# Kernel tuning notes

Hardware: AMD Instinct MI355X
Metric: run time of the kernel (lower is better)

Reference implementation:

```python
import jax, jax.numpy as jnp
import numpy as np

N = 100000
E = 1600000
IN_F = 128
HIDDEN = 128
HEADS = 2
N_CLASSES = 40
NEG_SLOPE = 0.2
BN_EPS = 1e-5


def setup_inputs() -> dict:
    key = jax.random.key(0)
    ks = jax.random.split(key, 12)
    c1 = HIDDEN // HEADS  # 64
    c2 = N_CLASSES        # 40 per head, concat=False
    inp = {
        "x": jax.random.normal(ks[0], (N, IN_F), dtype=jnp.float32),
        "edge_index": jax.random.randint(ks[1], (2, E), 0, N, dtype=jnp.int32),
        # layer 1 GATConv params
        "W1": jax.random.normal(ks[2], (IN_F, HEADS * c1), dtype=jnp.float32) * 0.05,
        "att_src1": jax.random.normal(ks[3], (HEADS, c1), dtype=jnp.float32) * 0.05,
        "att_dst1": jax.random.normal(ks[4], (HEADS, c1), dtype=jnp.float32) * 0.05,
        "b1": jnp.zeros((HEADS * c1,), dtype=jnp.float32),
        # BatchNorm params
        "gamma": jnp.ones((HIDDEN,), dtype=jnp.float32),
        "beta": jnp.zeros((HIDDEN,), dtype=jnp.float32),
        # layer 2 GATConv params (concat=False)
        "W2": jax.random.normal(ks[5], (HIDDEN, HEADS * c2), dtype=jnp.float32) * 0.05,
        "att_src2": jax.random.normal(ks[6], (HEADS, c2), dtype=jnp.float32) * 0.05,
        "att_dst2": jax.random.normal(ks[7], (HEADS, c2), dtype=jnp.float32) * 0.05,
        "b2": jnp.zeros((c2,), dtype=jnp.float32),
    }
    return inp


def gat_conv(x, src, dst, W, att_src, att_dst, bias, heads, concat):
    n = x.shape[0]
    h = (x @ W).reshape(n, heads, -1)             # [N, H, C]
    a_src = jnp.sum(h * att_src[None], axis=-1)   # [N, H]
    a_dst = jnp.sum(h * att_dst[None], axis=-1)   # [N, H]
    alpha = jax.nn.leaky_relu(a_src[src] + a_dst[dst], NEG_SLOPE)  # [E, H]
    # numerically-stable segment softmax over edges grouped by dst
    amax = jax.ops.segment_max(alpha, dst, num_segments=n)
    e = jnp.exp(alpha - amax[dst])
    denom = jax.ops.segment_sum(e, dst, num_segments=n)
    w = e / denom[dst]                            # [E, H]
    msg = h[src] * w[:, :, None]                  # [E, H, C]
    out = jax.ops.segment_sum(msg, dst, num_segments=n)  # [N, H, C]
    if concat:
        out = out.reshape(n, -1)
    else:
        out = out.mean(axis=1)
    return out + bias


def batch_norm(x, gamma, beta):
    mean = x.mean(axis=0)
    var = x.var(axis=0)
    return (x - mean) * jax.lax.rsqrt(var + BN_EPS) * gamma + beta


def reference(x, edge_index, W1, att_src1, att_dst1, b1, gamma, beta,
              W2, att_src2, att_dst2, b2):
    n = x.shape[0]
    # PyG GATConv default: add self-loops
    loops = jnp.arange(n, dtype=edge_index.dtype)
    src = jnp.concatenate([edge_index[0], loops])
    dst = jnp.concatenate([edge_index[1], loops])
    h = gat_conv(x, src, dst, W1, att_src1, att_dst1, b1, HEADS, concat=True)
    h = batch_norm(h, gamma, beta)
    h = gat_conv(h, src, dst, W2, att_src2, att_dst2, b2, HEADS, concat=False)
    return jax.nn.log_softmax(h, axis=1)
```

## Files before the change

### kernel.cpp

```cpp
#include <hip/hip_runtime.h>
#include <hip/hip_bf16.h>
#include <hip/hip_fp16.h>
#include <stdint.h>

#define N_NODES 100000
#define N_EDGES 1600000
#define ET (N_EDGES + N_NODES)
#define HID 128
#define C2 40
#define F2 80
#define NEG 0.2f
#define BN_EPS 1e-5f
#define NBUCK 391
#define BCAP 6144
#define NBB 640
#define EPB ((ET + NBB - 1) / NBB)

typedef __hip_bfloat16 bf16;
typedef __attribute__((ext_vector_type(8))) short s8v;
typedef __attribute__((ext_vector_type(4))) float f4v;
typedef __attribute__((ext_vector_type(4))) unsigned int u4v;
typedef __attribute__((ext_vector_type(2))) unsigned int u2v;

__device__ __forceinline__ float b2f(bf16 v){ return __bfloat162float(v); }
__device__ __forceinline__ float rdf(const void* p, size_t i, int isb){
    return isb ? b2f(((const bf16*)p)[i]) : ((const float*)p)[i];
}
__device__ __forceinline__ unsigned short f2bb(float v){
    bf16 h = __float2bfloat16(v);
    return *(unsigned short*)&h;
}
__device__ __forceinline__ uint32_t pack2(float a, float b){
    return (uint32_t)f2bb(a) | ((uint32_t)f2bb(b) << 16);
}
__device__ __forceinline__ float lo16(uint32_t u){ return __uint_as_float(u << 16); }
__device__ __forceinline__ float hi16(uint32_t u){ return __uint_as_float(u & 0xFFFF0000u); }
__device__ __forceinline__ float hcvt(uint32_t w, int sh){
    return __half2float(__ushort_as_half((unsigned short)((w >> sh) & 0xFFFFu)));
}

__global__ __launch_bounds__(256) void k_detect(
    const uint32_t* __restrict__ w1bits, int* __restrict__ flag)
{
    __shared__ int cnt;
    int t = threadIdx.x;
    if (t == 0) cnt = 0;
    __syncthreads();
    uint32_t b = w1bits[t];
    float lo = __uint_as_float((b & 0xFFFFu) << 16);
    float a = fabsf(lo);
    if (a > 1e-8f && a < 1.0f) atomicAdd(&cnt, 1);
    __syncthreads();
    if (t == 0) *flag = (cnt >= 192) ? 1 : 0;
}

__global__ __launch_bounds__(256) void k_gemm1(
    const void* __restrict__ x, const void* __restrict__ W1,
    const void* __restrict__ attS, const void* __restrict__ attD,
    const int* __restrict__ flag, unsigned short* __restrict__ h1,
    float* __restrict__ aS, float* __restrict__ aD)
{
    __shared__ __attribute__((aligned(16))) unsigned short wT[128*132];
    const int isb = *flag;
    const int tid = threadIdx.x;
    if (isb) {
        const unsigned short* w = (const unsigned short*)W1;
        for (int idx = tid; idx < 128*128; idx += 256){
            int k = idx >> 7, n = idx & 127;
            wT[n*132 + k] = w[idx];
        }
    } else {
        const float* w = (const float*)W1;
        for (int idx = tid; idx < 128*128; idx += 256){
            int k = idx >> 7, n = idx & 127;
            wT[n*132 + k] = f2bb(w[idx]);
        }
    }
    __syncthreads();

    const int w4 = tid >> 6, lane = tid & 63, quad = lane >> 4, l16 = lane & 15;
    const int rowbase = blockIdx.x*32 + (w4 >> 1)*16;
    const int colbase = (w4 & 1)*64;
    const int head = w4 & 1;

    s8v bfr[4][4];
    float asv[4], adv[4];
    #pragma unroll
    for (int ct = 0; ct < 4; ct++){
        int n = colbase + ct*16 + l16;
        asv[ct] = rdf(attS, n, isb);
        adv[ct] = rdf(attD, n, isb);
        #pragma unroll
        for (int s = 0; s < 4; s++){
            int k0 = s*32 + quad*8;
            const unsigned short* p = &wT[n*132 + k0];
            u2v a = *(const u2v*)p, b = *(const u2v*)(p+4);
            union { u4v u; s8v s; } cv; cv.u = (u4v){a[0],a[1],b[0],b[1]};
            bfr[ct][s] = cv.s;
        }
    }

    f4v acc[4];
    #pragma unroll
    for (int ct = 0; ct < 4; ct++) acc[ct] = (f4v){0.f,0.f,0.f,0.f};

    const int m = rowbase + l16;
    #pragma unroll
    for (int s = 0; s < 4; s++){
        int k0 = s*32 + quad*8;
        s8v af;
        if (isb){
            union { u4v u; s8v s; } cv;
            cv.u = *(const u4v*)((const unsigned short*)x + (size_t)m*128 + k0);
            af = cv.s;
        } else {
            const float* xp = (const float*)x + (size_t)m*128 + k0;
            f4v f0 = *(const f4v*)xp, f1 = *(const f4v*)(xp+4);
            union { u4v u; s8v s; } cv;
            cv.u = (u4v){pack2(f0[0],f0[1]), pack2(f0[2],f0[3]),
                         pack2(f1[0],f1[1]), pack2(f1[2],f1[3])};
            af = cv.s;
        }
        #pragma unroll
        for (int ct = 0; ct < 4; ct++)
            acc[ct] = __builtin_amdgcn_mfma_f32_16x16x32_bf16(af, bfr[ct][s], acc[ct], 0,0,0);
    }

    #pragma unroll
    for (int ct = 0; ct < 4; ct++){
        int col = colbase + ct*16 + l16;
        #pragma unroll
        for (int r = 0; r < 4; r++){
            int row = rowbase + quad*4 + r;
            h1[(size_t)row*128 + col] = f2bb(acc[ct][r]);
        }
    }

    #pragma unroll
    for (int r = 0; r < 4; r++){
        float vs = 0.f, vd = 0.f;
        #pragma unroll
        for (int ct = 0; ct < 4; ct++){ vs += acc[ct][r]*asv[ct]; vd += acc[ct][r]*adv[ct]; }
        #pragma unroll
        for (int o = 1; o < 16; o <<= 1){
            vs += __shfl_xor(vs, o, 64);
            vd += __shfl_xor(vd, o, 64);
        }
        if (l16 == 0){
            int row = rowbase + quad*4 + r;
            aS[row*2 + head] = vs;
            aD[row*2 + head] = vd;
        }
    }
}

__global__ __launch_bounds__(256) void k_bin(
    const int* __restrict__ esrc, const int* __restrict__ edst,
    int* __restrict__ gcur, uint32_t* __restrict__ staging)
{
    __shared__ int cnt[NBUCK];
    __shared__ int bb[NBUCK];
    const int t = threadIdx.x;
    for (int i = t; i < NBUCK; i += 256) cnt[i] = 0;
    __syncthreads();
    const int e0 = blockIdx.x * EPB;
    const int e1 = (e0 + EPB < ET) ? e0 + EPB : ET;
    for (int e = e0 + t; e < e1; e += 256){
        int d = (e < N_EDGES) ? edst[e] : e - N_EDGES;
        atomicAdd(&cnt[d >> 8], 1);
    }
    __syncthreads();
    const int bofs = (int)(blockIdx.x % NBUCK);
    for (int i = t; i < NBUCK; i += 256){
        int bkt = i + bofs; if (bkt >= NBUCK) bkt -= NBUCK;
        int c = cnt[bkt];
        bb[bkt] = c ? atomicAdd(&gcur[bkt], c) : 0;
        cnt[bkt] = 0;
    }
    __syncthreads();
    for (int e = e0 + t; e < e1; e += 256){
        int d, s;
        if (e < N_EDGES){ s = esrc[e]; d = edst[e]; } else { s = d = e - N_EDGES; }
        int b = d >> 8;
        int r = atomicAdd(&cnt[b], 1);
        int p = bb[b] + r;
        if (p < BCAP) staging[(size_t)b*BCAP + p] = ((uint32_t)s << 8) | (uint32_t)(d & 255);
    }
}

__global__ __launch_bounds__(256) void k_sort(
    const int* __restrict__ gcur, const uint32_t* __restrict__ staging,
    int* __restrict__ deg, int* __restrict__ cur, int* __restrict__ eidx)
{
    __shared__ int h[256], sc[256], rk[256];
    __shared__ int lsrc[BCAP];
    const int b = blockIdx.x;
    const int t = threadIdx.x;
    const int base = b * BCAP;
    int cnt = gcur[b];
    if (cnt > BCAP) cnt = BCAP;
    h[t] = 0; rk[t] = 0;
    __syncthreads();
    for (int i = t; i < cnt; i += 256)
        atomicAdd(&h[staging[base + i] & 255u], 1);
    __syncthreads();
    sc[t] = h[t];
    __syncthreads();
    for (int off = 1; off < 256; off <<= 1){
        int v = (t >= off) ? sc[t - off] : 0;
        __syncthreads();
        sc[t] += v;
        __syncthreads();
    }
    int dg = b*256 + t;
    if (dg < N_NODES){
        deg[dg] = h[t];
        cur[dg] = base + sc[t];
    }
    __syncthreads();
    for (int i = t; i < cnt; i += 256){
        uint32_t w = staging[base + i];
        int dl = w & 255u;
        int r = atomicAdd(&rk[dl], 1);
        lsrc[sc[dl] - h[dl] + r] = (int)(w >> 8);
    }
    __syncthreads();
    for (int i = t; i < cnt; i += 256) eidx[base + i] = lsrc[i];
}

__global__ __launch_bounds__(256) void k_ew(
    const int* __restrict__ cur, const int* __restrict__ deg,
    const int* __restrict__ eidx, const float* __restrict__ aS,
    const float* __restrict__ aD, uint32_t* __restrict__ wgt)
{
    int d = blockIdx.x*4 + (threadIdx.x >> 6);
    if (d >= N_NODES) return;
    int l = threadIdx.x & 63;
    int end   = __builtin_amdgcn_readfirstlane(cur[d]);
    int start = end - __builtin_amdgcn_readfirstlane(deg[d]);
    float2 ad = *(const float2*)(aD + d*2);
    float den0 = 0.f, den1 = 0.f;
    for (int j0 = start; j0 < end; j0 += 64){
        int j = j0 + l;
        float e0 = 0.f, e1 = 0.f;
        if (j < end){
            int s = eidx[j];
            float2 as = *(const float2*)(aS + s*2);
            float al0 = as.x + ad.x, al1 = as.y + ad.y;
            al0 = al0 > 0.f ? al0 : NEG*al0;
            al1 = al1 > 0.f ? al1 : NEG*al1;
            e0 = __expf(al0); e1 = __expf(al1);
        }
        den0 += e0; den1 += e1;
    }
    #pragma unroll
    for (int o = 1; o < 64; o <<= 1){
        den0 += __shfl_xor(den0, o, 64);
        den1 += __shfl_xor(den1, o, 64);
    }
    float i0 = 1.f / fmaxf(den0, 1e-20f);
    float i1 = 1.f / fmaxf(den1, 1e-20f);
    for (int j0 = start; j0 < end; j0 += 64){
        int j = j0 + l;
        if (j < end){
            int s = eidx[j];
            float2 as = *(const float2*)(aS + s*2);
            float al0 = as.x + ad.x, al1 = as.y + ad.y;
            al0 = al0 > 0.f ? al0 : NEG*al0;
            al1 = al1 > 0.f ? al1 : NEG*al1;
            unsigned short p0 = __half_as_ushort(__float2half(__expf(al0) * i0));
            unsigned short p1 = __half_as_ushort(__float2half(__expf(al1) * i1));
            wgt[j] = (uint32_t)p0 | ((uint32_t)p1 << 16);
        }
    }
}

__global__ __launch_bounds__(256) void k_agg1(
    const int* __restrict__ cur, const int* __restrict__ deg,
    const int* __restrict__ eidx, const uint32_t* __restrict__ wgt,
    const uint32_t* __restrict__ h1u, uint32_t* __restrict__ out1u)
{
    int d = blockIdx.x*4 + (threadIdx.x >> 6);
    if (d >= N_NODES) return;
    int l = threadIdx.x & 63;
    int end = __builtin_amdgcn_readfirstlane(cur[d]);
    int j   = end - __builtin_amdgcn_readfirstlane(deg[d]);
    const int sh = (l >= 32) ? 16 : 0;
    float acc0 = 0.f, acc1 = 0.f;

#define P1(W, G) { float Wf = hcvt(W, sh); \
    acc0 += Wf * lo16(G); acc1 += Wf * hi16(G); }

    for (; j + 4 <= end; j += 4){
        int s0 = eidx[j], s1 = eidx[j+1], s2 = eidx[j+2], s3 = eidx[j+3];
        uint32_t w0 = wgt[j], w1 = wgt[j+1], w2 = wgt[j+2], w3 = wgt[j+3];
        uint32_t g0 = h1u[(size_t)s0*64 + l];
        uint32_t g1 = h1u[(size_t)s1*64 + l];
        uint32_t g2 = h1u[(size_t)s2*64 + l];
        uint32_t g3 = h1u[(size_t)s3*64 + l];
        P1(w0, g0); P1(w1, g1); P1(w2, g2); P1(w3, g3);
    }
    for (; j < end; j++){
        int s = eidx[j];
        uint32_t w = wgt[j];
        uint32_t g = h1u[(size_t)s*64 + l];
        P1(w, g);
    }
#undef P1
    out1u[(size_t)d*64 + l] = pack2(acc0, acc1);
}

__global__ __launch_bounds__(256) void k_bnstats(
    const uint32_t* __restrict__ out1u, float* __restrict__ stats)
{
    __shared__ float red[4][64][4];
    int fp = threadIdx.x & 63;
    int wv = threadIdx.x >> 6;
    float s0 = 0.f, q0 = 0.f, s1 = 0.f, q1 = 0.f;
    for (int r = blockIdx.x*4 + wv; r < N_NODES; r += 512){
        uint32_t u = out1u[(size_t)r*64 + fp];
        float f0 = lo16(u), f1 = hi16(u);
        s0 += f0; q0 += f0*f0; s1 += f1; q1 += f1*f1;
    }
    red[wv][fp][0] = s0; red[wv][fp][1] = s1;
    red[wv][fp][2] = q0; red[wv][fp][3] = q1;
    __syncthreads();
    if (threadIdx.x < 64){
        int l = threadIdx.x;
        float a0=0.f, a1=0.f, b0=0.f, b1=0.f;
        #pragma unroll
        for (int w = 0; w < 4; w++){
            a0 += red[w][l][0]; a1 += red[w][l][1];
            b0 += red[w][l][2]; b1 += red[w][l][3];
        }
        unsafeAtomicAdd(&stats[2*l],       a0);
        unsafeAtomicAdd(&stats[2*l+1],     a1);
        unsafeAtomicAdd(&stats[128+2*l],   b0);
        unsafeAtomicAdd(&stats[128+2*l+1], b1);
    }
}

__global__ __launch_bounds__(256) void k_gemm2(
    const unsigned short* __restrict__ out1b, const float* __restrict__ stats,
    const void* __restrict__ gamma, const void* __restrict__ beta,
    const void* __restrict__ W2, const void* __restrict__ attS,
    const void* __restrict__ attD, const int* __restrict__ flag,
    unsigned short* __restrict__ h2, float* __restrict__ aS, float* __restrict__ aD)
{
    __shared__ __attribute__((aligned(16))) unsigned short wT[80*132];
    __shared__ float scl[128], shl[128];
    const int isb = *flag;
    const int tid = threadIdx.x;
    for (int idx = tid; idx < 128*80; idx += 256){
        int k = idx / 80, n = idx - k*80;
        wT[n*132 + k] = isb ? ((const unsigned short*)W2)[idx]
                            : f2bb(((const float*)W2)[idx]);
    }
    if (tid < 128){
        float mean = stats[tid] * (1.f / N_NODES);
        float var = fmaxf(stats[128+tid] * (1.f / N_NODES) - mean*mean, 0.f);
        float rs = rsqrtf(var + BN_EPS);
        float sc = rdf(gamma, tid, isb) * rs;
        scl[tid] = sc;
        shl[tid] = rdf(beta, tid, isb) - mean*sc;
    }
    __syncthreads();

    const int w4 = tid >> 6, lane = tid & 63, quad = lane >> 4, l16 = lane & 15;
    const int rowbase = blockIdx.x*64 + w4*16;

    s8v bfr[5][4];
    float asv[5], adv[5];
    #pragma unroll
    for (int ct = 0; ct < 5; ct++){
        int n = ct*16 + l16;
        asv[ct] = rdf(attS, n, isb);
        adv[ct] = rdf(attD, n, isb);
        #pragma unroll
        for (int s = 0; s < 4; s++){
            int k0 = s*32 + quad*8;
            const unsigned short* p = &wT[n*132 + k0];
            u2v a = *(const u2v*)p, b = *(const u2v*)(p+4);
            union { u4v u; s8v s; } cv; cv.u = (u4v){a[0],a[1],b[0],b[1]};
            bfr[ct][s] = cv.s;
        }
    }

    f4v acc[5];
    #pragma unroll
    for (int ct = 0; ct < 5; ct++) acc[ct] = (f4v){0.f,0.f,0.f,0.f};

    int m = rowbase + l16;
    int mc = m < N_NODES ? m : N_NODES - 1;
    #pragma unroll
    for (int s = 0; s < 4; s++){
        int k0 = s*32 + quad*8;
        union { u4v u; s8v s8; } cin;
        cin.u = *(const u4v*)(out1b + (size_t)mc*128 + k0);
        u4v up;
        #pragma unroll
        for (int i = 0; i < 4; i++){
            float f0 = lo16(cin.u[i]), f1 = hi16(cin.u[i]);
            int k = k0 + 2*i;
            up[i] = pack2(f0*scl[k] + shl[k], f1*scl[k+1] + shl[k+1]);
        }
        union { u4v u; s8v s8; } cv; cv.u = up;
        #pragma unroll
        for (int ct = 0; ct < 5; ct++)
            acc[ct] = __builtin_amdgcn_mfma_f32_16x16x32_bf16(cv.s8, bfr[ct][s], acc[ct], 0,0,0);
    }

    #pragma unroll
    for (int ct = 0; ct < 5; ct++){
        int col = ct*16 + l16;
        #pragma unroll
        for (int r = 0; r < 4; r++){
            int row = rowbase + quad*4 + r;
            if (row < N_NODES) h2[(size_t)row*80 + col] = f2bb(acc[ct][r]);
        }
    }

    #pragma unroll
    for (int r = 0; r < 4; r++){
        float vs0 = 0.f, vs1 = 0.f, vd0 = 0.f, vd1 = 0.f;
        #pragma unroll
        for (int ct = 0; ct < 5; ct++){
            int col = ct*16 + l16;
            float ps = acc[ct][r]*asv[ct], pd = acc[ct][r]*adv[ct];
            if (col < 40){ vs0 += ps; vd0 += pd; } else { vs1 += ps; vd1 += pd; }
        }
        #pragma unroll
        for (int o = 1; o < 16; o <<= 1){
            vs0 += __shfl_xor(vs0, o, 64); vs1 += __shfl_xor(vs1, o, 64);
            vd0 += __shfl_xor(vd0, o, 64); vd1 += __shfl_xor(vd1, o, 64);
        }
        if (l16 == 0){
            int row = rowbase + quad*4 + r;
            if (row < N_NODES){
                aS[row*2 + 0] = vs0; aS[row*2 + 1] = vs1;
                aD[row*2 + 0] = vd0; aD[row*2 + 1] = vd1;
            }
        }
    }
}

__global__ __launch_bounds__(256) void k_agg2(
    const int* __restrict__ cur, const int* __restrict__ deg,
    const int* __restrict__ eidx, const uint32_t* __restrict__ wgt,
    const uint32_t* __restrict__ h2u, const void* __restrict__ b2v,
    const int* __restrict__ flag, void* __restrict__ out)
{
    int d = blockIdx.x*4 + (threadIdx.x >> 6);
    if (d >= N_NODES) return;
    int l = threadIdx.x & 63;
    if (l >= 40) return;
    const int isb = *flag;
    int end = __builtin_amdgcn_readfirstlane(cur[d]);
    int j   = end - __builtin_amdgcn_readfirstlane(deg[d]);
    const int sh = (l >= 20) ? 16 : 0;
    float acc0 = 0.f, acc1 = 0.f;

#define P2(W, G) { float Wf = hcvt(W, sh); \
    acc0 += Wf * lo16(G); acc1 += Wf * hi16(G); }

    for (; j + 4 <= end; j += 4){
        int s0 = eidx[j], s1 = eidx[j+1], s2 = eidx[j+2], s3 = eidx[j+3];
        uint32_t w0 = wgt[j], w1 = wgt[j+1], w2 = wgt[j+2], w3 = wgt[j+3];
        uint32_t g0 = h2u[(size_t)s0*40 + l];
        uint32_t g1 = h2u[(size_t)s1*40 + l];
        uint32_t g2 = h2u[(size_t)s2*40 + l];
        uint32_t g3 = h2u[(size_t)s3*40 + l];
        P2(w0, g0); P2(w1, g1); P2(w2, g2); P2(w3, g3);
    }
    for (; j < end; j++){
        int s = eidx[j];
        uint32_t w = wgt[j];
        uint32_t g = h2u[(size_t)s*40 + l];
        P2(w, g);
    }
#undef P2

    float m0 = 0.5f*(acc0 + __shfl(acc0, l + 20, 64));
    float m1 = 0.5f*(acc1 + __shfl(acc1, l + 20, 64));
    float v0 = -1e30f, v1 = -1e30f;
    if (l < 20){
        v0 = m0 + rdf(b2v, 2*l,   isb);
        v1 = m1 + rdf(b2v, 2*l+1, isb);
    }
    float mx = fmaxf(v0, v1);
    #pragma unroll
    for (int o = 1; o < 32; o <<= 1) mx = fmaxf(mx, __shfl_xor(mx, o, 64));
    float ex = (l < 20) ? __expf(v0 - mx) + __expf(v1 - mx) : 0.f;
    #pragma unroll
    for (int o = 1; o < 32; o <<= 1) ex += __shfl_xor(ex, o, 64);
    float lse = __logf(ex);
    if (l < 20){
        float r0 = v0 - mx - lse, r1 = v1 - mx - lse;
        if (isb){
            ((uint32_t*)out)[(size_t)d*20 + l] = pack2(r0, r1);
        } else {
            float2 wr; wr.x = r0; wr.y = r1;
            ((float2*)out)[(size_t)d*20 + l] = wr;
        }
    }
}

extern "C" void kernel_launch(void* const* d_in, const int* in_sizes, int n_in,
                              void* d_out, int out_size, void* d_ws, size_t ws_size,
                              hipStream_t stream)
{
    const void* x    = d_in[0];
    const int*  ei   = (const int*)d_in[1];
    const void* W1   = d_in[2];
    const void* as1  = d_in[3];
    const void* ad1  = d_in[4];
    const void* gamma = d_in[6];
    const void* beta  = d_in[7];
    const void* W2   = d_in[8];
    const void* as2  = d_in[9];
    const void* ad2  = d_in[10];
    const void* b2v  = d_in[11];
    const int* esrc = ei;
    const int* edst = ei + N_EDGES;

    char* ws = (char*)d_ws;
    size_t off = 0;
    auto alloc = [&](size_t bytes) {
        void* p = ws + off;
        off += (bytes + 255) & ~(size_t)255;
        return p;
    };
    int*   flag  = (int*)alloc(256);
    float* stats = (float*)alloc(sizeof(float)*256);
    int*   gcur  = (int*)alloc(sizeof(int)*NBUCK);
    float* aS1   = (float*)alloc(sizeof(float)*N_NODES*2);
    float* aD1   = (float*)alloc(sizeof(float)*N_NODES*2);
    float* aS2   = (float*)alloc(sizeof(float)*N_NODES*2);
    float* aD2   = (float*)alloc(sizeof(float)*N_NODES*2);
    int*   deg   = (int*)alloc(sizeof(int)*N_NODES);
    int*   cur   = (int*)alloc(sizeof(int)*N_NODES);
    uint32_t* staging = (uint32_t*)alloc(sizeof(uint32_t)*(size_t)NBUCK*BCAP);
    int*   eidx  = (int*)alloc(sizeof(int)*(size_t)NBUCK*BCAP);
    unsigned short* h1  = (unsigned short*)alloc(2*(size_t)N_NODES*HID);
    unsigned short* out1 = (unsigned short*)alloc(2*(size_t)N_NODES*HID);
    unsigned short* h2  = h1;
    uint32_t* wgt = staging;

    hipMemsetAsync(gcur, 0, sizeof(int)*NBUCK, stream);
    hipMemsetAsync(stats, 0, sizeof(float)*256, stream);

    k_detect<<<1, 256, 0, stream>>>((const uint32_t*)W1, flag);
    k_gemm1<<<3125, 256, 0, stream>>>(x, W1, as1, ad1, flag, h1, aS1, aD1);
    k_bin<<<NBB, 256, 0, stream>>>(esrc, edst, gcur, staging);
    k_sort<<<NBUCK, 256, 0, stream>>>(gcur, staging, deg, cur, eidx);
    k_ew<<<25000, 256, 0, stream>>>(cur, deg, eidx, aS1, aD1, wgt);
    k_agg1<<<25000, 256, 0, stream>>>(cur, deg, eidx, wgt,
                                      (const uint32_t*)h1, (uint32_t*)out1);
    k_bnstats<<<128, 256, 0, stream>>>((const uint32_t*)out1, stats);
    k_gemm2<<<1563, 256, 0, stream>>>(out1, stats, gamma, beta, W2, as2, ad2,
                                      flag, h2, aS2, aD2);
    k_ew<<<25000, 256, 0, stream>>>(cur, deg, eidx, aS2, aD2, wgt);
    k_agg2<<<25000, 256, 0, stream>>>(cur, deg, eidx, wgt,
                                      (const uint32_t*)h2, b2v, flag, d_out);
}
```

Before: 478.5 us.

## Fuse edge-weight softmax into aggregation kernels via LDS staging and deferred normalization

Removes the separate edge-weight kernel and computes unnormalized exp scores inside each aggregation kernel. The scores are staged in shared memory together with the source index, and the accumulated result is divided by the softmax denominator at the end. This drops two launches, the weight-array write and read, and a second pass over the edges. The memset calls are also folded into the detect kernel. In exchange each kernel now holds 16KB of LDS per block, which can lower occupancy, and unnormalized exps stored in fp16 could overflow for large logits.

New measurement: 437.4 us. 8.6% less time.

```diff
diff --git a/kernel.cpp b/kernel.cpp
--- a/kernel.cpp
+++ b/kernel.cpp
@@ -15,6 +15,7 @@
 #define BCAP 6144
 #define NBB 640
 #define EPB ((ET + NBB - 1) / NBB)
+#define CHK 512
 
 typedef __hip_bfloat16 bf16;
 typedef __attribute__((ext_vector_type(8))) short s8v;
@@ -33,14 +34,19 @@
 __device__ __forceinline__ uint32_t pack2(float a, float b){
     return (uint32_t)f2bb(a) | ((uint32_t)f2bb(b) << 16);
 }
+__device__ __forceinline__ uint32_t packh2(float a, float b){
+    return (uint32_t)__half_as_ushort(__float2half(a))
+         | ((uint32_t)__half_as_ushort(__float2half(b)) << 16);
+}
 __device__ __forceinline__ float lo16(uint32_t u){ return __uint_as_float(u << 16); }
 __device__ __forceinline__ float hi16(uint32_t u){ return __uint_as_float(u & 0xFFFF0000u); }
 __device__ __forceinline__ float hcvt(uint32_t w, int sh){
     return __half2float(__ushort_as_half((unsigned short)((w >> sh) & 0xFFFFu)));
 }
 
-__global__ __launch_bounds__(256) void k_detect(
-    const uint32_t* __restrict__ w1bits, int* __restrict__ flag)
+__global__ __launch_bounds__(256) void k_init(
+    const uint32_t* __restrict__ w1bits, int* __restrict__ flag,
+    int* __restrict__ gcur, float* __restrict__ stats)
 {
     __shared__ int cnt;
     int t = threadIdx.x;
@@ -50,6 +56,8 @@
     float lo = __uint_as_float((b & 0xFFFFu) << 16);
     float a = fabsf(lo);
     if (a > 1e-8f && a < 1.0f) atomicAdd(&cnt, 1);
+    for (int i = t; i < NBUCK; i += 256) gcur[i] = 0;
+    stats[t] = 0.f;
     __syncthreads();
     if (t == 0) *flag = (cnt >= 192) ? 1 : 0;
 }
@@ -228,86 +236,55 @@
     for (int i = t; i < cnt; i += 256) eidx[base + i] = lsrc[i];
 }
 
-__global__ __launch_bounds__(256) void k_ew(
+__global__ __launch_bounds__(256) void k_agg1(
     const int* __restrict__ cur, const int* __restrict__ deg,
     const int* __restrict__ eidx, const float* __restrict__ aS,
-    const float* __restrict__ aD, uint32_t* __restrict__ wgt)
-{
-    int d = blockIdx.x*4 + (threadIdx.x >> 6);
+    const float* __restrict__ aD, const uint32_t* __restrict__ h1u,
+    uint32_t* __restrict__ out1u)
+{
+    __shared__ uint2 lse[4][CHK];
+    const int wv = threadIdx.x >> 6;
+    int d = blockIdx.x*4 + wv;
     if (d >= N_NODES) return;
-    int l = threadIdx.x & 63;
+    const int l = threadIdx.x & 63;
     int end   = __builtin_amdgcn_readfirstlane(cur[d]);
     int start = end - __builtin_amdgcn_readfirstlane(deg[d]);
     float2 ad = *(const float2*)(aD + d*2);
-    float den0 = 0.f, den1 = 0.f;
-    for (int j0 = start; j0 < end; j0 += 64){
-        int j = j0 + l;
-        float e0 = 0.f, e1 = 0.f;
-        if (j < end){
+    const int sh = (l >= 32) ? 16 : 0;
+    float den0 = 0.f, den1 = 0.f, acc0 = 0.f, acc1 = 0.f;
+
+#define P1(P) { float Wf = hcvt((P).y, sh); uint32_t G = h1u[(size_t)(P).x*64 + l]; \
+    acc0 += Wf * lo16(G); acc1 += Wf * hi16(G); }
+
+    for (int c0 = start; c0 < end; c0 += CHK){
+        int c1 = (c0 + CHK < end) ? c0 + CHK : end;
+        int n = c1 - c0;
+        for (int j = c0 + l; j < c1; j += 64){
             int s = eidx[j];
             float2 as = *(const float2*)(aS + s*2);
             float al0 = as.x + ad.x, al1 = as.y + ad.y;
             al0 = al0 > 0.f ? al0 : NEG*al0;
             al1 = al1 > 0.f ? al1 : NEG*al1;
-            e0 = __expf(al0); e1 = __expf(al1);
-        }
-        den0 += e0; den1 += e1;
-    }
+            float e0 = __expf(al0), e1 = __expf(al1);
+            lse[wv][j - c0] = make_uint2((uint32_t)s, packh2(e0, e1));
+            den0 += e0; den1 += e1;
+        }
+        int i = 0;
+        for (; i + 4 <= n; i += 4){
+            uint2 p0 = lse[wv][i],   p1 = lse[wv][i+1];
+            uint2 p2 = lse[wv][i+2], p3 = lse[wv][i+3];
+            P1(p0); P1(p1); P1(p2); P1(p3);
+        }
+        for (; i < n; i++){ uint2 p = lse[wv][i]; P1(p); }
+    }
+#undef P1
     #pragma unroll
     for (int o = 1; o < 64; o <<= 1){
         den0 += __shfl_xor(den0, o, 64);
         den1 += __shfl_xor(den1, o, 64);
     }
-    float i0 = 1.f / fmaxf(den0, 1e-20f);
-    float i1 = 1.f / fmaxf(den1, 1e-20f);
-    for (int j0 = start; j0 < end; j0 += 64){
-        int j = j0 + l;
-        if (j < end){
-            int s = eidx[j];
-            float2 as = *(const float2*)(aS + s*2);
-            float al0 = as.x + ad.x, al1 = as.y + ad.y;
-            al0 = al0 > 0.f ? al0 : NEG*al0;
-            al1 = al1 > 0.f ? al1 : NEG*al1;
-            unsigned short p0 = __half_as_ushort(__float2half(__expf(al0) * i0));
-            unsigned short p1 = __half_as_ushort(__float2half(__expf(al1) * i1));
-            wgt[j] = (uint32_t)p0 | ((uint32_t)p1 << 16);
-        }
-    }
-}
-
-__global__ __launch_bounds__(256) void k_agg1(
-    const int* __restrict__ cur, const int* __restrict__ deg,
-    const int* __restrict__ eidx, const uint32_t* __restrict__ wgt,
-    const uint32_t* __restrict__ h1u, uint32_t* __restrict__ out1u)
-{
-    int d = blockIdx.x*4 + (threadIdx.x >> 6);
-    if (d >= N_NODES) return;
-    int l = threadIdx.x & 63;
-    int end = __builtin_amdgcn_readfirstlane(cur[d]);
-    int j   = end - __builtin_amdgcn_readfirstlane(deg[d]);
-    const int sh = (l >= 32) ? 16 : 0;
-    float acc0 = 0.f, acc1 = 0.f;
-
-#define P1(W, G) { float Wf = hcvt(W, sh); \
-    acc0 += Wf * lo16(G); acc1 += Wf * hi16(G); }
-
-    for (; j + 4 <= end; j += 4){
-        int s0 = eidx[j], s1 = eidx[j+1], s2 = eidx[j+2], s3 = eidx[j+3];
-        uint32_t w0 = wgt[j], w1 = wgt[j+1], w2 = wgt[j+2], w3 = wgt[j+3];
-        uint32_t g0 = h1u[(size_t)s0*64 + l];
-        uint32_t g1 = h1u[(size_t)s1*64 + l];
-        uint32_t g2 = h1u[(size_t)s2*64 + l];
-        uint32_t g3 = h1u[(size_t)s3*64 + l];
-        P1(w0, g0); P1(w1, g1); P1(w2, g2); P1(w3, g3);
-    }
-    for (; j < end; j++){
-        int s = eidx[j];
-        uint32_t w = wgt[j];
-        uint32_t g = h1u[(size_t)s*64 + l];
-        P1(w, g);
-    }
-#undef P1
-    out1u[(size_t)d*64 + l] = pack2(acc0, acc1);
+    float r = 1.f / fmaxf((l < 32) ? den0 : den1, 1e-20f);
+    out1u[(size_t)d*64 + l] = pack2(acc0*r, acc1*r);
 }
 
 __global__ __launch_bounds__(256) void k_bnstats(
@@ -446,39 +423,57 @@
 
 __global__ __launch_bounds__(256) void k_agg2(
     const int* __restrict__ cur, const int* __restrict__ deg,
-    const int* __restrict__ eidx, const uint32_t* __restrict__ wgt,
-    const uint32_t* __restrict__ h2u, const void* __restrict__ b2v,
-    const int* __restrict__ flag, void* __restrict__ out)
-{
-    int d = blockIdx.x*4 + (threadIdx.x >> 6);
+    const int* __restrict__ eidx, const float* __restrict__ aS,
+    const float* __restrict__ aD, const uint32_t* __restrict__ h2u,
+    const void* __restrict__ b2v, const int* __restrict__ flag,
+    void* __restrict__ out)
+{
+    __shared__ uint2 lse[4][CHK];
+    const int wv = threadIdx.x >> 6;
+    int d = blockIdx.x*4 + wv;
     if (d >= N_NODES) return;
-    int l = threadIdx.x & 63;
-    if (l >= 40) return;
+    const int l = threadIdx.x & 63;
     const int isb = *flag;
-    int end = __builtin_amdgcn_readfirstlane(cur[d]);
-    int j   = end - __builtin_amdgcn_readfirstlane(deg[d]);
+    int end   = __builtin_amdgcn_readfirstlane(cur[d]);
+    int start = end - __builtin_amdgcn_readfirstlane(deg[d]);
+    float2 ad = *(const float2*)(aD + d*2);
     const int sh = (l >= 20) ? 16 : 0;
-    float acc0 = 0.f, acc1 = 0.f;
-
-#define P2(W, G) { float Wf = hcvt(W, sh); \
+    const bool act = l < 40;
+    float den0 = 0.f, den1 = 0.f, acc0 = 0.f, acc1 = 0.f;
+
+#define P2(P) { float Wf = hcvt((P).y, sh); \
+    uint32_t G = act ? h2u[(size_t)(P).x*40 + l] : 0u; \
     acc0 += Wf * lo16(G); acc1 += Wf * hi16(G); }
 
-    for (; j + 4 <= end; j += 4){
-        int s0 = eidx[j], s1 = eidx[j+1], s2 = eidx[j+2], s3 = eidx[j+3];
-        uint32_t w0 = wgt[j], w1 = wgt[j+1], w2 = wgt[j+2], w3 = wgt[j+3];
-        uint32_t g0 = h2u[(size_t)s0*40 + l];
-        uint32_t g1 = h2u[(size_t)s1*40 + l];
-        uint32_t g2 = h2u[(size_t)s2*40 + l];
-        uint32_t g3 = h2u[(size_t)s3*40 + l];
-        P2(w0, g0); P2(w1, g1); P2(w2, g2); P2(w3, g3);
-    }
-    for (; j < end; j++){
-        int s = eidx[j];
-        uint32_t w = wgt[j];
-        uint32_t g = h2u[(size_t)s*40 + l];
-        P2(w, g);
+    for (int c0 = start; c0 < end; c0 += CHK){
+        int c1 = (c0 + CHK < end) ? c0 + CHK : end;
+        int n = c1 - c0;
+        for (int j = c0 + l; j < c1; j += 64){
+            int s = eidx[j];
+            float2 as = *(const float2*)(aS + s*2);
+            float al0 = as.x + ad.x, al1 = as.y + ad.y;
+            al0 = al0 > 0.f ? al0 : NEG*al0;
+            al1 = al1 > 0.f ? al1 : NEG*al1;
+            float e0 = __expf(al0), e1 = __expf(al1);
+            lse[wv][j - c0] = make_uint2((uint32_t)s, packh2(e0, e1));
+            den0 += e0; den1 += e1;
+        }
+        int i = 0;
+        for (; i + 4 <= n; i += 4){
+            uint2 p0 = lse[wv][i],   p1 = lse[wv][i+1];
+            uint2 p2 = lse[wv][i+2], p3 = lse[wv][i+3];
+            P2(p0); P2(p1); P2(p2); P2(p3);
+        }
+        for (; i < n; i++){ uint2 p = lse[wv][i]; P2(p); }
     }
 #undef P2
+    #pragma unroll
+    for (int o = 1; o < 64; o <<= 1){
+        den0 += __shfl_xor(den0, o, 64);
+        den1 += __shfl_xor(den1, o, 64);
+    }
+    float r = 1.f / fmaxf((l < 20) ? den0 : den1, 1e-20f);
+    acc0 *= r; acc1 *= r;
 
     float m0 = 0.5f*(acc0 + __shfl(acc0, l + 20, 64));
     float m1 = 0.5f*(acc1 + __shfl(acc1, l + 20, 64));
@@ -493,9 +488,9 @@
     float ex = (l < 20) ? __expf(v0 - mx) + __expf(v1 - mx) : 0.f;
     #pragma unroll
     for (int o = 1; o < 32; o <<= 1) ex += __shfl_xor(ex, o, 64);
-    float lse = __logf(ex);
+    float lse2 = __logf(ex);
     if (l < 20){
-        float r0 = v0 - mx - lse, r1 = v1 - mx - lse;
+        float r0 = v0 - mx - lse2, r1 = v1 - mx - lse2;
         if (isb){
             ((uint32_t*)out)[(size_t)d*20 + l] = pack2(r0, r1);
         } else {
@@ -544,22 +539,16 @@
     unsigned short* h1  = (unsigned short*)alloc(2*(size_t)N_NODES*HID);
     unsigned short* out1 = (unsigned short*)alloc(2*(size_t)N_NODES*HID);
     unsigned short* h2  = h1;
-    uint32_t* wgt = staging;
-
-    hipMemsetAsync(gcur, 0, sizeof(int)*NBUCK, stream);
-    hipMemsetAsync(stats, 0, sizeof(float)*256, stream);
-
-    k_detect<<<1, 256, 0, stream>>>((const uint32_t*)W1, flag);
+
+    k_init<<<1, 256, 0, stream>>>((const uint32_t*)W1, flag, gcur, stats);
     k_gemm1<<<3125, 256, 0, stream>>>(x, W1, as1, ad1, flag, h1, aS1, aD1);
     k_bin<<<NBB, 256, 0, stream>>>(esrc, edst, gcur, staging);
     k_sort<<<NBUCK, 256, 0, stream>>>(gcur, staging, deg, cur, eidx);
-    k_ew<<<25000, 256, 0, stream>>>(cur, deg, eidx, aS1, aD1, wgt);
-    k_agg1<<<25000, 256, 0, stream>>>(cur, deg, eidx, wgt,
+    k_agg1<<<25000, 256, 0, stream>>>(cur, deg, eidx, aS1, aD1,
                                       (const uint32_t*)h1, (uint32_t*)out1);
     k_bnstats<<<128, 256, 0, stream>>>((const uint32_t*)out1, stats);
     k_gemm2<<<1563, 256, 0, stream>>>(out1, stats, gamma, beta, W2, as2, ad2,
                                       flag, h2, aS2, aD2);
-    k_ew<<<25000, 256, 0, stream>>>(cur, deg, eidx, aS2, aD2, wgt);
-    k_agg2<<<25000, 256, 0, stream>>>(cur, deg, eidx, wgt,
+    k_agg2<<<25000, 256, 0, stream>>>(cur, deg, eidx, aS2, aD2,
                                       (const uint32_t*)h2, b2v, flag, d_out);
 }
```
